# Kernel optimization log

Hardware: AMD Instinct MI355X
Metric: run time of the kernel (lower is better)

Reference implementation:

```python
import jax, jax.numpy as jnp
import numpy as np

B, C, Dz, Hh, Ww = 1, 128, 24, 24, 24
L = Dz * Hh * Ww
D_STATE = 16
D_CONV = 4
EXPAND = 2
D_INNER = EXPAND * C
DT_RANK = (C + 15) // 16  # ceil(d_model/16) = 8


def setup_inputs() -> dict:
    key = jax.random.key(0)
    ks = jax.random.split(key, 10)
    s = 0.02
    return {
        "x": jax.random.normal(ks[0], (B, C, Dz, Hh, Ww), dtype=jnp.float32),
        "ln_w": jnp.ones((C,), jnp.float32),
        "ln_b": jnp.zeros((C,), jnp.float32),
        "in_proj_w": s * jax.random.normal(ks[1], (2 * D_INNER, C), jnp.float32),
        "conv_w": s * jax.random.normal(ks[2], (D_INNER, D_CONV), jnp.float32),
        "conv_b": jnp.zeros((D_INNER,), jnp.float32),
        "x_proj_w": s * jax.random.normal(ks[3], (DT_RANK + 2 * D_STATE, D_INNER), jnp.float32),
        "dt_proj_w": s * jax.random.normal(ks[4], (D_INNER, DT_RANK), jnp.float32),
        "dt_proj_b": jax.random.uniform(ks[5], (D_INNER,), jnp.float32, -4.0, -2.0),
        "A_log": jnp.log(jnp.broadcast_to(jnp.arange(1, D_STATE + 1, dtype=jnp.float32), (D_INNER, D_STATE))),
        "D_param": jnp.ones((D_INNER,), jnp.float32),
        "out_proj_w": s * jax.random.normal(ks[6], (C, D_INNER), jnp.float32),
    }


def _mamba_forward(x, ln_w, ln_b, in_proj_w, conv_w, conv_b, x_proj_w,
                   dt_proj_w, dt_proj_b, A_log, D_param, out_proj_w):
    b, c, d, h, w = x.shape
    l = d * h * w
    tokens = x.reshape(b, c, l).transpose(0, 2, 1)  # (B,L,C)

    # LayerNorm over channel dim
    mu = jnp.mean(tokens, axis=-1, keepdims=True)
    var = jnp.var(tokens, axis=-1, keepdims=True)
    tn = (tokens - mu) * jax.lax.rsqrt(var + 1e-5) * ln_w + ln_b

    # in_proj -> x, z
    xz = jnp.einsum('blc,ec->ble', tn, in_proj_w)  # (B,L,2*d_inner)
    xs, z = jnp.split(xz, 2, axis=-1)

    # causal depthwise conv1d over L (kernel size D_CONV)
    xpad = jnp.pad(xs, ((0, 0), (D_CONV - 1, 0), (0, 0)))
    xc = conv_b
    xc = sum(xpad[:, k:k + l, :] * conv_w[:, k] for k in range(D_CONV)) + conv_b
    xa = jax.nn.silu(xc)  # (B,L,d_inner)

    # x_proj -> dt, B, C
    x_dbl = jnp.einsum('bld,ed->ble', xa, x_proj_w)
    dt_in = x_dbl[..., :DT_RANK]
    Bm = x_dbl[..., DT_RANK:DT_RANK + D_STATE]          # (B,L,d_state)
    Cm = x_dbl[..., DT_RANK + D_STATE:]                 # (B,L,d_state)
    dt = jax.nn.softplus(jnp.einsum('blr,dr->bld', dt_in, dt_proj_w) + dt_proj_b)

    A = -jnp.exp(A_log)  # (d_inner, d_state)

    def step(hst, inp):
        dt_t, B_t, C_t, x_t = inp  # (B,d_inner),(B,d_state),(B,d_state),(B,d_inner)
        dA = jnp.exp(dt_t[..., None] * A)                       # (B,d_inner,d_state)
        hst = dA * hst + (dt_t * x_t)[..., None] * B_t[:, None, :]
        y_t = jnp.einsum('bds,bs->bd', hst, C_t)
        return hst, y_t

    h0 = jnp.zeros((b, D_INNER, D_STATE), xa.dtype)
    xs_t = (dt.transpose(1, 0, 2), Bm.transpose(1, 0, 2), Cm.transpose(1, 0, 2), xa.transpose(1, 0, 2))
    _, ys = jax.lax.scan(step, h0, xs_t)
    y = ys.transpose(1, 0, 2) + xa * D_param  # (B,L,d_inner)

    y = y * jax.nn.silu(z)
    out = jnp.einsum('bld,cd->blc', y, out_proj_w)

    tokens = tokens + out
    return tokens.transpose(0, 2, 1).reshape(b, c, d, h, w)


def reference(x, ln_w, ln_b, in_proj_w, conv_w, conv_b, x_proj_w,
              dt_proj_w, dt_proj_b, A_log, D_param, out_proj_w):
    return _mamba_forward(x, ln_w, ln_b, in_proj_w, conv_w, conv_b, x_proj_w,
                          dt_proj_w, dt_proj_b, A_log, D_param, out_proj_w)
```

## Files before the change

### kernel.cpp

```cpp
#include <hip/hip_runtime.h>
#include <hip/hip_bf16.h>
#include <math.h>


constexpr int LQ = 13824;
constexpr int NC = 108;
constexpr int CH = 128;
constexpr int DI = 256;
constexpr int DS = 16;

typedef __attribute__((ext_vector_type(8))) short short8v;
typedef __attribute__((ext_vector_type(4))) float float4v;

__device__ __forceinline__ ushort f2bf(float f) {
  uint u = __float_as_uint(f);
  u += 0x7FFFu + ((u >> 16) & 1u);
  return (ushort)(u >> 16);
}
__device__ __forceinline__ float bf2f(ushort u) {
  return __uint_as_float(((uint)u) << 16);
}

template<int CTRL>
__device__ __forceinline__ float dpp_add(float x) {
  int y = __builtin_amdgcn_update_dpp(0, __float_as_int(x), CTRL, 0xF, 0xF, true);
  return x + __int_as_float(y);
}
__device__ __forceinline__ float dpp_reduce16(float t) {
  t = dpp_add<0xB1>(t);
  t = dpp_add<0x4E>(t);
  t = dpp_add<0x141>(t);
  t = dpp_add<0x140>(t);
  return t;
}

__global__ __launch_bounds__(256) void prep_w2(const float* __restrict__ w_in,
    const float* __restrict__ w_xp, const float* __restrict__ w_dt,
    const float* __restrict__ w_out,
    ushort* __restrict__ b_in, ushort* __restrict__ b_xp2, ushort* __restrict__ b_out) {
  int idx = blockIdx.x * 256 + threadIdx.x;
  if (idx < 65536) {
    b_in[idx] = f2bf(w_in[idx]);
  } else if (idx < 65536 + 8192) {
    int j = idx - 65536; int r = j >> 8, k = j & 255;
    b_xp2[j] = f2bf(w_xp[(8 + r) * 256 + k]);
  } else if (idx < 65536 + 8192 + 65536) {
    int j = idx - (65536 + 8192); int d = j >> 8, k = j & 255;
    float acc = 0.f;
    #pragma unroll
    for (int r = 0; r < 8; ++r) acc += w_dt[d * 8 + r] * w_xp[r * 256 + k];
    b_xp2[8192 + j] = f2bf(acc);
  } else if (idx < 65536 + 8192 + 65536 + 8192) {
    b_xp2[73728 + (idx - 139264)] = 0;
  } else if (idx < 180224) {
    int j = idx - 147456;
    b_out[j] = f2bf(w_out[j]);
  }
}

__global__ __launch_bounds__(256) void ln_t(const float* __restrict__ x,
    const float* __restrict__ lnw, const float* __restrict__ lnb,
    ushort* __restrict__ tn) {
  __shared__ float red[64][8];
  __shared__ float stat[64][2];
  __shared__ ushort T[64][136];
  const int t = threadIdx.x;
  const int l = t & 63, q = t >> 6;
  const int l0 = blockIdx.x * 64;
  float sum = 0.f, sq = 0.f;
  #pragma unroll 8
  for (int cc = 0; cc < 32; ++cc) {
    int c = q * 32 + cc;
    float v = x[(size_t)c * LQ + l0 + l];
    sum += v; sq += v * v;
  }
  red[l][q] = sum; red[l][4 + q] = sq;
  __syncthreads();
  if (t < 64) {
    float s  = red[t][0] + red[t][1] + red[t][2] + red[t][3];
    float s2 = red[t][4] + red[t][5] + red[t][6] + red[t][7];
    float mu = s * (1.f / 128.f);
    float var = s2 * (1.f / 128.f) - mu * mu;
    stat[t][0] = mu; stat[t][1] = rsqrtf(var + 1e-5f);
  }
  __syncthreads();
  float mu = stat[l][0], rs = stat[l][1];
  #pragma unroll 8
  for (int cc = 0; cc < 32; ++cc) {
    int c = q * 32 + cc;
    float v = x[(size_t)c * LQ + l0 + l];
    T[l][c] = f2bf((v - mu) * rs * lnw[c] + lnb[c]);
  }
  __syncthreads();
  int row = t >> 2, seg = t & 3;
  #pragma unroll
  for (int j = 0; j < 4; ++j) {
    short8v v = *(const short8v*)&T[row][seg * 32 + j * 8];
    *(short8v*)&tn[(size_t)(l0 + row) * 128 + seg * 32 + j * 8] = v;
  }
}

template<int K, int MV, int BSTR, int CSTR>
__global__ __launch_bounds__(256) void gemm_tok(
    const ushort* __restrict__ Wb,
    const ushort* __restrict__ Act,
    ushort* __restrict__ Out) {
  constexpr int KO = K / 8;
  __shared__ ushort As[64 * K];
  __shared__ ushort Bs[128 * 64];
  const int tid = threadIdx.x;
  const int l0 = blockIdx.x * 128;
  const int m0 = blockIdx.y * 64;
  #pragma unroll
  for (int i = 0; i < (64 * KO) / 256; ++i) {
    int cid = i * 256 + tid;
    int m = cid / KO, oct = cid % KO;
    short8v v = *(const short8v*)&Wb[(size_t)(m0 + m) * K + oct * 8];
    *(short8v*)&As[m * K + ((oct ^ (m & 7)) * 8)] = v;
  }
  float4v acc[4][2];
  #pragma unroll
  for (int a = 0; a < 4; ++a)
    #pragma unroll
    for (int b = 0; b < 2; ++b) acc[a][b] = (float4v)0.f;
  const int w = tid >> 6, lane = tid & 63;
  const int r = lane & 15, g = lane >> 4;
  for (int k0 = 0; k0 < K; k0 += 64) {
    __syncthreads();
    #pragma unroll
    for (int i = 0; i < 4; ++i) {
      int cid = i * 256 + tid;
      int l = cid >> 3, oct = cid & 7;
      short8v v = *(const short8v*)&Act[(size_t)(l0 + l) * BSTR + k0 + oct * 8];
      *(short8v*)&Bs[l * 64 + ((oct ^ (l & 7)) * 8)] = v;
    }
    __syncthreads();
    #pragma unroll
    for (int kk = 0; kk < 2; ++kk) {
      short8v af[4], bfv[2];
      int ko = (k0 >> 3) + kk * 4 + g;
      #pragma unroll
      for (int mf = 0; mf < 4; ++mf) {
        int row = mf * 16 + r;
        af[mf] = *(const short8v*)&As[row * K + ((ko ^ (row & 7)) * 8)];
      }
      int kob = kk * 4 + g;
      #pragma unroll
      for (int nf = 0; nf < 2; ++nf) {
        int row = w * 32 + nf * 16 + r;
        bfv[nf] = *(const short8v*)&Bs[row * 64 + ((kob ^ (row & 7)) * 8)];
      }
      #pragma unroll
      for (int mf = 0; mf < 4; ++mf)
        #pragma unroll
        for (int nf = 0; nf < 2; ++nf)
          acc[mf][nf] = __builtin_amdgcn_mfma_f32_16x16x32_bf16(af[mf], bfv[nf], acc[mf][nf], 0, 0, 0);
    }
  }
  __syncthreads();
  #pragma unroll
  for (int mf = 0; mf < 4; ++mf) {
    #pragma unroll
    for (int nf = 0; nf < 2; ++nf) {
      int l = w * 32 + nf * 16 + r;
      int m = mf * 16 + g * 4;
      ushort u0 = f2bf(acc[mf][nf][0]), u1 = f2bf(acc[mf][nf][1]);
      ushort u2 = f2bf(acc[mf][nf][2]), u3 = f2bf(acc[mf][nf][3]);
      uint2 pk = make_uint2((uint)u0 | ((uint)u1 << 16), (uint)u2 | ((uint)u3 << 16));
      int oct = (m >> 3) ^ (l & 7);
      *(uint2*)&Bs[l * 64 + oct * 8 + (g & 1) * 4] = pk;
    }
  }
  __syncthreads();
  #pragma unroll
  for (int i = 0; i < 4; ++i) {
    int cid = i * 256 + tid;
    int row = cid >> 3, oct = cid & 7;
    if (oct * 8 < MV) {
      short8v v = *(const short8v*)&Bs[row * 64 + ((oct ^ (row & 7)) * 8)];
      *(short8v*)&Out[(size_t)(l0 + row) * CSTR + m0 + oct * 8] = v;
    }
  }
}

__global__ __launch_bounds__(256) void gemm_out_k(
    const ushort* __restrict__ Wb,
    const ushort* __restrict__ Yg,
    const float* __restrict__ X,
    float* __restrict__ Out) {
  __shared__ ushort Ay[128 * 64];
  __shared__ ushort Bw[128 * 64];
  const int tid = threadIdx.x;
  const int l0 = blockIdx.x * 128;
  const int w = tid >> 6, lane = tid & 63;
  const int r = lane & 15, g = lane >> 4;
  const int lw = w >> 1, cw = w & 1;
  float4v acc[4][4];
  #pragma unroll
  for (int a = 0; a < 4; ++a)
    #pragma unroll
    for (int b = 0; b < 4; ++b) acc[a][b] = (float4v)0.f;
  for (int k0 = 0; k0 < 256; k0 += 64) {
    __syncthreads();
    #pragma unroll
    for (int i = 0; i < 4; ++i) {
      int cid = i * 256 + tid;
      int row = cid >> 3, oct = cid & 7;
      int k = k0 + oct * 8;
      int slab = k >> 4, rem = k & 15;
      short8v va = *(const short8v*)&Yg[((size_t)slab * LQ + l0 + row) * 16 + rem];
      *(short8v*)&Ay[row * 64 + ((oct ^ (row & 7)) * 8)] = va;
      short8v vb = *(const short8v*)&Wb[(size_t)row * 256 + k0 + oct * 8];
      *(short8v*)&Bw[row * 64 + ((oct ^ (row & 7)) * 8)] = vb;
    }
    __syncthreads();
    #pragma unroll
    for (int kk = 0; kk < 2; ++kk) {
      int ko = kk * 4 + g;
      short8v af[4], bfv[4];
      #pragma unroll
      for (int mf = 0; mf < 4; ++mf) {
        int row = lw * 64 + mf * 16 + r;
        af[mf] = *(const short8v*)&Ay[row * 64 + ((ko ^ (row & 7)) * 8)];
      }
      #pragma unroll
      for (int nf = 0; nf < 4; ++nf) {
        int row = cw * 64 + nf * 16 + r;
        bfv[nf] = *(const short8v*)&Bw[row * 64 + ((ko ^ (row & 7)) * 8)];
      }
      #pragma unroll
      for (int mf = 0; mf < 4; ++mf)
        #pragma unroll
        for (int nf = 0; nf < 4; ++nf)
          acc[mf][nf] = __builtin_amdgcn_mfma_f32_16x16x32_bf16(af[mf], bfv[nf], acc[mf][nf], 0, 0, 0);
    }
  }
  #pragma unroll
  for (int mf = 0; mf < 4; ++mf) {
    #pragma unroll
    for (int nf = 0; nf < 4; ++nf) {
      int c = cw * 64 + nf * 16 + r;
      int l = l0 + lw * 64 + mf * 16 + g * 4;
      size_t off = (size_t)c * LQ + l;
      float4 rv = *(const float4*)&X[off];
      float4 o = make_float4(acc[mf][nf][0] + rv.x, acc[mf][nf][1] + rv.y,
                             acc[mf][nf][2] + rv.z, acc[mf][nf][3] + rv.w);
      *(float4*)&Out[off] = o;
    }
  }
}

__global__ __launch_bounds__(256) void conv2(const ushort* __restrict__ xz,
    const float* __restrict__ cw, const float* __restrict__ cb,
    ushort* __restrict__ xa) {
  const int tid = threadIdx.x;
  const int d0 = (tid & 31) * 8;
  const int l0 = blockIdx.x * 32 + (tid >> 5) * 4;
  float w0[8], w1[8], w2[8], w3[8], bb[8];
  #pragma unroll
  for (int j = 0; j < 8; ++j) {
    float4 wv = *(const float4*)&cw[(d0 + j) * 4];
    w0[j] = wv.x; w1[j] = wv.y; w2[j] = wv.z; w3[j] = wv.w;
    bb[j] = cb[d0 + j];
  }
  float rbuf[7][8];
  #pragma unroll
  for (int t = 0; t < 7; ++t) {
    int ls = l0 - 3 + t;
    if (ls >= 0) {
      short8v v = *(const short8v*)&xz[(size_t)ls * 512 + d0];
      #pragma unroll
      for (int j = 0; j < 8; ++j) rbuf[t][j] = bf2f((ushort)v[j]);
    } else {
      #pragma unroll
      for (int j = 0; j < 8; ++j) rbuf[t][j] = 0.f;
    }
  }
  #pragma unroll
  for (int i = 0; i < 4; ++i) {
    short8v ov;
    #pragma unroll
    for (int j = 0; j < 8; ++j) {
      float acc = bb[j] + w0[j] * rbuf[i][j] + w1[j] * rbuf[i + 1][j]
                        + w2[j] * rbuf[i + 2][j] + w3[j] * rbuf[i + 3][j];
      ov[j] = (short)f2bf(acc / (1.f + __expf(-acc)));
    }
    *(short8v*)&xa[(size_t)(l0 + i) * 256 + d0] = ov;
  }
}

__global__ __launch_bounds__(256) void scan1(const ushort* __restrict__ xdbl,
    const ushort* __restrict__ xa, const float* __restrict__ bias,
    const float* __restrict__ A_log, float* __restrict__ Pc, float* __restrict__ Hc,
    ushort* __restrict__ yloc) {
  __shared__ uint  duL[128 * 17];
  __shared__ ushort bcL[128 * 40];
  __shared__ float ylds[128 * 18];
  const int tid = threadIdx.x;
  const int c = blockIdx.x, dg = blockIdx.y;
  const int l0 = c * CH;
  {
    const int row = tid >> 1, half = tid & 1;
    const ushort* xr = xdbl + (size_t)(l0 + row) * 320;
    short8v dl = *(const short8v*)(xr + 32 + dg * 16 + half * 8);
    short8v xv = *(const short8v*)(&xa[(size_t)(l0 + row) * 256 + dg * 16 + half * 8]);
    #pragma unroll
    for (int j = 0; j < 8; ++j) {
      float av = bf2f((ushort)dl[j]) + bias[dg * 16 + half * 8 + j];
      float sp = (av > 20.f) ? av : log1pf(__expf(av));
      float dx = sp * bf2f((ushort)xv[j]);
      duL[row * 17 + half * 8 + j] = (uint)f2bf(sp) | ((uint)f2bf(dx) << 16);
    }
    short8v bv = *(const short8v*)(xr + half * 8);
    short8v cv = *(const short8v*)(xr + 16 + half * 8);
    uint* bcu = (uint*)bcL;
    #pragma unroll
    for (int j = 0; j < 4; ++j) {
      bcu[row * 20 + half * 4 + j] =
          (uint)(ushort)bv[2 * j] | ((uint)(ushort)bv[2 * j + 1] << 16);
      bcu[row * 20 + 8 + half * 4 + j] =
          (uint)(ushort)cv[2 * j] | ((uint)(ushort)cv[2 * j + 1] << 16);
    }
  }
  __syncthreads();
  const int s = tid & 15, dloc = tid >> 4;
  const int d = dg * 16 + dloc;
  const float A = -__expf(A_log[d * DS + s]);
  float p = 1.f, h = 0.f;
  #pragma unroll 4
  for (int i = 0; i < CH; ++i) {
    uint pv = duL[i * 17 + dloc];
    float dtv = bf2f((ushort)(pv & 0xffffu));
    float dx  = bf2f((ushort)(pv >> 16));
    float a = __expf(dtv * A);
    p *= a;
    h = fmaf(a, h, dx * bf2f(bcL[i * 40 + s]));
    float t = dpp_reduce16(h * bf2f(bcL[i * 40 + 16 + s]));
    if (s == 0) ylds[i * 18 + dloc] = t;
  }
  int idx = (c * DI + d) * DS + s;
  Pc[idx] = p; Hc[idx] = h;
  __syncthreads();
  {
    const int row = tid >> 1, half = tid & 1;
    short8v ov;
    #pragma unroll
    for (int j = 0; j < 8; ++j) ov[j] = (short)f2bf(ylds[row * 18 + half * 8 + j]);
    *(short8v*)&yloc[((size_t)dg * LQ + l0 + row) * 16 + half * 8] = ov;
  }
}

__global__ __launch_bounds__(256) void scan_combine(const float* __restrict__ Pc,
    const float* __restrict__ Hc, float* __restrict__ Hin) {
  int t = blockIdx.x * 256 + threadIdx.x;
  float h = 0.f;
  for (int c = 0; c < NC; ++c) {
    Hin[c * 4096 + t] = h;
    h = Pc[c * 4096 + t] * h + Hc[c * 4096 + t];
  }
}

__global__ __launch_bounds__(256) void scan2(const ushort* __restrict__ xdbl,
    const ushort* __restrict__ xa, const ushort* __restrict__ xz,
    const float* __restrict__ bias, const float* __restrict__ A_log,
    const float* __restrict__ Dp, const float* __restrict__ Hin,
    ushort* __restrict__ yg) {
  __shared__ ushort dtL[128 * 18];
  __shared__ ushort cL[128 * 18];
  __shared__ float corr[128 * 18];
  const int tid = threadIdx.x;
  const int c = blockIdx.x, dg = blockIdx.y;
  const int l0 = c * CH;
  {
    const int row = tid >> 1, half = tid & 1;
    const ushort* xr = xdbl + (size_t)(l0 + row) * 320;
    short8v dl = *(const short8v*)(xr + 32 + dg * 16 + half * 8);
    short8v cv = *(const short8v*)(xr + 16 + half * 8);
    uint* dtu = (uint*)dtL;
    uint* cu  = (uint*)cL;
    ushort sp8[8];
    #pragma unroll
    for (int j = 0; j < 8; ++j) {
      float av = bf2f((ushort)dl[j]) + bias[dg * 16 + half * 8 + j];
      float sp = (av > 20.f) ? av : log1pf(__expf(av));
      sp8[j] = f2bf(sp);
    }
    #pragma unroll
    for (int j = 0; j < 4; ++j) {
      dtu[row * 9 + half * 4 + j] = (uint)sp8[2 * j] | ((uint)sp8[2 * j + 1] << 16);
      cu[row * 9 + half * 4 + j] =
          (uint)(ushort)cv[2 * j] | ((uint)(ushort)cv[2 * j + 1] << 16);
    }
  }
  __syncthreads();
  const int s = tid & 15, dloc = tid >> 4;
  const int d = dg * 16 + dloc;
  const float A = -__expf(A_log[d * DS + s]);
  const float hin = Hin[c * 4096 + d * DS + s];
  float S = 0.f;
  #pragma unroll 4
  for (int i = 0; i < CH; ++i) {
    S += bf2f(dtL[i * 18 + dloc]);
    float e = __expf(A * S);
    float t = dpp_reduce16((hin * e) * bf2f(cL[i * 18 + s]));
    if (s == 0) corr[i * 18 + dloc] = t;
  }
  __syncthreads();
  {
    const int row = tid >> 1, half = tid & 1;
    const size_t slab = ((size_t)dg * LQ + l0 + row) * 16 + half * 8;
    short8v yl = *(const short8v*)&yg[slab];
    short8v xv = *(const short8v*)&xa[(size_t)(l0 + row) * 256 + dg * 16 + half * 8];
    short8v zv = *(const short8v*)&xz[(size_t)(l0 + row) * 512 + 256 + dg * 16 + half * 8];
    short8v ov;
    #pragma unroll
    for (int j = 0; j < 8; ++j) {
      float val = bf2f((ushort)yl[j]) + corr[row * 18 + half * 8 + j]
                + bf2f((ushort)xv[j]) * Dp[dg * 16 + half * 8 + j];
      float zf = bf2f((ushort)zv[j]);
      val *= zf / (1.f + __expf(-zf));
      ov[j] = (short)f2bf(val);
    }
    *(short8v*)&yg[slab] = ov;
  }
}

extern "C" void kernel_launch(void* const* d_in, const int* in_sizes, int n_in,
                              void* d_out, int out_size, void* d_ws, size_t ws_size,
                              hipStream_t stream) {
  const float* x         = (const float*)d_in[0];
  const float* ln_w      = (const float*)d_in[1];
  const float* ln_b      = (const float*)d_in[2];
  const float* in_proj_w = (const float*)d_in[3];
  const float* conv_w    = (const float*)d_in[4];
  const float* conv_b    = (const float*)d_in[5];
  const float* x_proj_w  = (const float*)d_in[6];
  const float* dt_proj_w = (const float*)d_in[7];
  const float* dt_proj_b = (const float*)d_in[8];
  const float* A_log     = (const float*)d_in[9];
  const float* D_param   = (const float*)d_in[10];
  const float* out_proj_w= (const float*)d_in[11];
  float* out = (float*)d_out;

  char* ws = (char*)d_ws;
  ushort* wbf_in  = (ushort*)(ws + 0);
  ushort* wbf_xp2 = (ushort*)(ws + 131072);
  ushort* wbf_out = (ushort*)(ws + 294912);
  float*  Hin     = (float*)(ws + 360448);
  ushort* tn_t    = (ushort*)(ws + 2129920);
  float*  Pc      = (float*)(ws + 2129920);
  float*  Hc      = (float*)(ws + 3899392);
  ushort* xz_t    = (ushort*)(ws + 5668864);
  ushort* xa_t    = (ushort*)(ws + 19824640);
  ushort* xdbl_t  = (ushort*)(ws + 26902528);
  ushort* yg_t    = (ushort*)(ws + 35749888);

  prep_w2<<<704, 256, 0, stream>>>(in_proj_w, x_proj_w, dt_proj_w, out_proj_w,
                                   wbf_in, wbf_xp2, wbf_out);
  ln_t<<<LQ / 64, 256, 0, stream>>>(x, ln_w, ln_b, tn_t);
  gemm_tok<128, 64, 128, 512><<<dim3(NC, 8), 256, 0, stream>>>(wbf_in, tn_t, xz_t);
  conv2<<<LQ / 32, 256, 0, stream>>>(xz_t, conv_w, conv_b, xa_t);
  gemm_tok<256, 64, 256, 320><<<dim3(NC, 5), 256, 0, stream>>>(wbf_xp2, xa_t, xdbl_t);
  scan1<<<dim3(NC, 16), 256, 0, stream>>>(xdbl_t, xa_t, dt_proj_b, A_log, Pc, Hc, yg_t);
  scan_combine<<<16, 256, 0, stream>>>(Pc, Hc, Hin);
  scan2<<<dim3(NC, 16), 256, 0, stream>>>(xdbl_t, xa_t, xz_t, dt_proj_b, A_log,
                                          D_param, Hin, yg_t);
  gemm_out_k<<<NC, 256, 0, stream>>>(wbf_out, yg_t, x, out);
}
```

Baseline: 207.2 us.

## Remap scan threads to four states per lane and split out-proj GEMM over channels

The chunked selective scan now gives each thread four state elements for one channel, so the cross-lane reduction needs only a quad DPP step instead of a 16-lane one. Each block covers 64 channels in two 64-step stages, and B/C are staged as fp32 in shared memory. The per-chunk decay product is replaced by a cumulative dt sum that scan_combine turns back into exp(A*S). The output GEMM is also split across two column blocks to double its grid. This trades fewer, larger scan blocks (432 instead of 1728) for less shuffle and LDS traffic per step, which may lower occupancy on the scan kernels.

```diff
diff --git a/kernel.cpp b/kernel.cpp
--- a/kernel.cpp
+++ b/kernel.cpp
@@ -26,12 +26,13 @@
   int y = __builtin_amdgcn_update_dpp(0, __float_as_int(x), CTRL, 0xF, 0xF, true);
   return x + __int_as_float(y);
 }
-__device__ __forceinline__ float dpp_reduce16(float t) {
+__device__ __forceinline__ float quad_reduce(float t) {
   t = dpp_add<0xB1>(t);
   t = dpp_add<0x4E>(t);
-  t = dpp_add<0x141>(t);
-  t = dpp_add<0x140>(t);
   return t;
+}
+__device__ __forceinline__ float softplus_f(float x) {
+  return (x > 20.f) ? x : log1pf(__expf(x));
 }
 
 __global__ __launch_bounds__(256) void prep_w2(const float* __restrict__ w_in,
@@ -189,15 +190,15 @@
     const float* __restrict__ X,
     float* __restrict__ Out) {
   __shared__ ushort Ay[128 * 64];
-  __shared__ ushort Bw[128 * 64];
+  __shared__ ushort Bw[64 * 64];
   const int tid = threadIdx.x;
   const int l0 = blockIdx.x * 128;
+  const int c0 = blockIdx.y * 64;
   const int w = tid >> 6, lane = tid & 63;
   const int r = lane & 15, g = lane >> 4;
-  const int lw = w >> 1, cw = w & 1;
-  float4v acc[4][4];
-  #pragma unroll
-  for (int a = 0; a < 4; ++a)
+  float4v acc[2][4];
+  #pragma unroll
+  for (int a = 0; a < 2; ++a)
     #pragma unroll
     for (int b = 0; b < 4; ++b) acc[a][b] = (float4v)0.f;
   for (int k0 = 0; k0 < 256; k0 += 64) {
@@ -210,37 +211,42 @@
       int slab = k >> 4, rem = k & 15;
       short8v va = *(const short8v*)&Yg[((size_t)slab * LQ + l0 + row) * 16 + rem];
       *(short8v*)&Ay[row * 64 + ((oct ^ (row & 7)) * 8)] = va;
-      short8v vb = *(const short8v*)&Wb[(size_t)row * 256 + k0 + oct * 8];
+    }
+    #pragma unroll
+    for (int i = 0; i < 2; ++i) {
+      int cid = i * 256 + tid;
+      int row = cid >> 3, oct = cid & 7;
+      short8v vb = *(const short8v*)&Wb[(size_t)(c0 + row) * 256 + k0 + oct * 8];
       *(short8v*)&Bw[row * 64 + ((oct ^ (row & 7)) * 8)] = vb;
     }
     __syncthreads();
     #pragma unroll
     for (int kk = 0; kk < 2; ++kk) {
       int ko = kk * 4 + g;
-      short8v af[4], bfv[4];
-      #pragma unroll
-      for (int mf = 0; mf < 4; ++mf) {
-        int row = lw * 64 + mf * 16 + r;
+      short8v af[2], bfv[4];
+      #pragma unroll
+      for (int mf = 0; mf < 2; ++mf) {
+        int row = w * 32 + mf * 16 + r;
         af[mf] = *(const short8v*)&Ay[row * 64 + ((ko ^ (row & 7)) * 8)];
       }
       #pragma unroll
       for (int nf = 0; nf < 4; ++nf) {
-        int row = cw * 64 + nf * 16 + r;
+        int row = nf * 16 + r;
         bfv[nf] = *(const short8v*)&Bw[row * 64 + ((ko ^ (row & 7)) * 8)];
       }
       #pragma unroll
-      for (int mf = 0; mf < 4; ++mf)
+      for (int mf = 0; mf < 2; ++mf)
         #pragma unroll
         for (int nf = 0; nf < 4; ++nf)
           acc[mf][nf] = __builtin_amdgcn_mfma_f32_16x16x32_bf16(af[mf], bfv[nf], acc[mf][nf], 0, 0, 0);
     }
   }
   #pragma unroll
-  for (int mf = 0; mf < 4; ++mf) {
+  for (int mf = 0; mf < 2; ++mf) {
     #pragma unroll
     for (int nf = 0; nf < 4; ++nf) {
-      int c = cw * 64 + nf * 16 + r;
-      int l = l0 + lw * 64 + mf * 16 + g * 4;
+      int c = c0 + nf * 16 + r;
+      int l = l0 + w * 32 + mf * 16 + g * 4;
       size_t off = (size_t)c * LQ + l;
       float4 rv = *(const float4*)&X[off];
       float4 o = make_float4(acc[mf][nf][0] + rv.x, acc[mf][nf][1] + rv.y,
@@ -291,72 +297,103 @@
 
 __global__ __launch_bounds__(256) void scan1(const ushort* __restrict__ xdbl,
     const ushort* __restrict__ xa, const float* __restrict__ bias,
-    const float* __restrict__ A_log, float* __restrict__ Pc, float* __restrict__ Hc,
+    const float* __restrict__ A_log, float* __restrict__ Stot, float* __restrict__ Hc,
     ushort* __restrict__ yloc) {
-  __shared__ uint  duL[128 * 17];
-  __shared__ ushort bcL[128 * 40];
-  __shared__ float ylds[128 * 18];
+  __shared__ uint  duL[64 * 64];
+  __shared__ float bcL[64 * 32];
+  __shared__ ushort ylds[64 * 72];
   const int tid = threadIdx.x;
   const int c = blockIdx.x, dg = blockIdx.y;
-  const int l0 = c * CH;
-  {
-    const int row = tid >> 1, half = tid & 1;
-    const ushort* xr = xdbl + (size_t)(l0 + row) * 320;
-    short8v dl = *(const short8v*)(xr + 32 + dg * 16 + half * 8);
-    short8v xv = *(const short8v*)(&xa[(size_t)(l0 + row) * 256 + dg * 16 + half * 8]);
-    #pragma unroll
-    for (int j = 0; j < 8; ++j) {
-      float av = bf2f((ushort)dl[j]) + bias[dg * 16 + half * 8 + j];
-      float sp = (av > 20.f) ? av : log1pf(__expf(av));
-      float dx = sp * bf2f((ushort)xv[j]);
-      duL[row * 17 + half * 8 + j] = (uint)f2bf(sp) | ((uint)f2bf(dx) << 16);
-    }
-    short8v bv = *(const short8v*)(xr + half * 8);
-    short8v cv = *(const short8v*)(xr + 16 + half * 8);
-    uint* bcu = (uint*)bcL;
-    #pragma unroll
-    for (int j = 0; j < 4; ++j) {
-      bcu[row * 20 + half * 4 + j] =
-          (uint)(ushort)bv[2 * j] | ((uint)(ushort)bv[2 * j + 1] << 16);
-      bcu[row * 20 + 8 + half * 4 + j] =
-          (uint)(ushort)cv[2 * j] | ((uint)(ushort)cv[2 * j + 1] << 16);
-    }
-  }
-  __syncthreads();
-  const int s = tid & 15, dloc = tid >> 4;
-  const int d = dg * 16 + dloc;
-  const float A = -__expf(A_log[d * DS + s]);
-  float p = 1.f, h = 0.f;
-  #pragma unroll 4
-  for (int i = 0; i < CH; ++i) {
-    uint pv = duL[i * 17 + dloc];
-    float dtv = bf2f((ushort)(pv & 0xffffu));
-    float dx  = bf2f((ushort)(pv >> 16));
-    float a = __expf(dtv * A);
-    p *= a;
-    h = fmaf(a, h, dx * bf2f(bcL[i * 40 + s]));
-    float t = dpp_reduce16(h * bf2f(bcL[i * 40 + 16 + s]));
-    if (s == 0) ylds[i * 18 + dloc] = t;
-  }
-  int idx = (c * DI + d) * DS + s;
-  Pc[idx] = p; Hc[idx] = h;
-  __syncthreads();
-  {
-    const int row = tid >> 1, half = tid & 1;
-    short8v ov;
-    #pragma unroll
-    for (int j = 0; j < 8; ++j) ov[j] = (short)f2bf(ylds[row * 18 + half * 8 + j]);
-    *(short8v*)&yloc[((size_t)dg * LQ + l0 + row) * 16 + half * 8] = ov;
-  }
-}
-
-__global__ __launch_bounds__(256) void scan_combine(const float* __restrict__ Pc,
-    const float* __restrict__ Hc, float* __restrict__ Hin) {
+  const int dloc = tid >> 2, sq = tid & 3;
+  const int d = dg * 64 + dloc;
+  float4v A, h;
+  #pragma unroll
+  for (int k = 0; k < 4; ++k) {
+    A[k] = -__expf(A_log[d * 16 + sq * 4 + k]);
+    h[k] = 0.f;
+  }
+  float S = 0.f;
+  for (int stg = 0; stg < 2; ++stg) {
+    const int lb = c * CH + stg * 64;
+    __syncthreads();
+    {
+      const int doff = dg * 64 + sq * 16;
+      const ushort* xr = xdbl + (size_t)(lb + dloc) * 320 + 32 + doff;
+      const ushort* xar = xa + (size_t)(lb + dloc) * 256 + doff;
+      short8v d0 = *(const short8v*)xr;
+      short8v d1 = *(const short8v*)(xr + 8);
+      short8v x0 = *(const short8v*)xar;
+      short8v x1 = *(const short8v*)(xar + 8);
+      uint pk[16];
+      #pragma unroll
+      for (int j = 0; j < 8; ++j) {
+        float sp = softplus_f(bf2f((ushort)d0[j]) + bias[doff + j]);
+        pk[j] = (uint)f2bf(sp) | ((uint)f2bf(sp * bf2f((ushort)x0[j])) << 16);
+        float sp2 = softplus_f(bf2f((ushort)d1[j]) + bias[doff + 8 + j]);
+        pk[8 + j] = (uint)f2bf(sp2) | ((uint)f2bf(sp2 * bf2f((ushort)x1[j])) << 16);
+      }
+      uint4* dst = (uint4*)&duL[dloc * 64 + sq * 16];
+      #pragma unroll
+      for (int j = 0; j < 4; ++j)
+        dst[j] = make_uint4(pk[4 * j], pk[4 * j + 1], pk[4 * j + 2], pk[4 * j + 3]);
+    }
+    if (tid < 128) {
+      int row = tid >> 1, half = tid & 1;
+      const ushort* xr = xdbl + (size_t)(lb + row) * 320;
+      short8v bv = *(const short8v*)(xr + half * 8);
+      short8v cv = *(const short8v*)(xr + 16 + half * 8);
+      float* bd = &bcL[row * 32 + half * 8];
+      float* cd = &bcL[row * 32 + 16 + half * 8];
+      #pragma unroll
+      for (int j = 0; j < 8; ++j) {
+        bd[j] = bf2f((ushort)bv[j]);
+        cd[j] = bf2f((ushort)cv[j]);
+      }
+    }
+    __syncthreads();
+    #pragma unroll 4
+    for (int i = 0; i < 64; ++i) {
+      uint pv = duL[i * 64 + dloc];
+      float dtv = __uint_as_float(pv << 16);
+      float dxv = __uint_as_float(pv & 0xffff0000u);
+      S += dtv;
+      float4v Bv = *(const float4v*)&bcL[i * 32 + sq * 4];
+      float4v Cv = *(const float4v*)&bcL[i * 32 + 16 + sq * 4];
+      float t = 0.f;
+      #pragma unroll
+      for (int k = 0; k < 4; ++k) {
+        float a = __expf(dtv * A[k]);
+        h[k] = fmaf(a, h[k], dxv * Bv[k]);
+        t = fmaf(h[k], Cv[k], t);
+      }
+      t = quad_reduce(t);
+      if (sq == 0) ylds[i * 72 + dloc] = f2bf(t);
+    }
+    __syncthreads();
+    {
+      int slab = tid >> 6, row = tid & 63;
+      short8v v0 = *(const short8v*)&ylds[row * 72 + slab * 16];
+      short8v v1 = *(const short8v*)&ylds[row * 72 + slab * 16 + 8];
+      ushort* dst = &yloc[((size_t)(dg * 4 + slab) * LQ + lb + row) * 16];
+      *(short8v*)dst = v0;
+      *(short8v*)(dst + 8) = v1;
+    }
+  }
+  *(float4*)&Hc[(size_t)(c * 256 + d) * 16 + sq * 4] = make_float4(h[0], h[1], h[2], h[3]);
+  if (sq == 0) Stot[c * 256 + d] = S;
+}
+
+__global__ __launch_bounds__(256) void scan_combine(const float* __restrict__ Stot,
+    const float* __restrict__ Hc, const float* __restrict__ A_log,
+    float* __restrict__ Hin) {
   int t = blockIdx.x * 256 + threadIdx.x;
+  int d = t >> 4;
+  float A = -__expf(A_log[t]);
   float h = 0.f;
   for (int c = 0; c < NC; ++c) {
     Hin[c * 4096 + t] = h;
-    h = Pc[c * 4096 + t] * h + Hc[c * 4096 + t];
+    float a = __expf(A * Stot[c * 256 + d]);
+    h = a * h + Hc[c * 4096 + t];
   }
 }
 
@@ -365,63 +402,99 @@
     const float* __restrict__ bias, const float* __restrict__ A_log,
     const float* __restrict__ Dp, const float* __restrict__ Hin,
     ushort* __restrict__ yg) {
-  __shared__ ushort dtL[128 * 18];
-  __shared__ ushort cL[128 * 18];
-  __shared__ float corr[128 * 18];
+  __shared__ uint  dtp[32 * 64];
+  __shared__ float cL[64 * 16];
+  __shared__ float corr[64 * 68];
   const int tid = threadIdx.x;
   const int c = blockIdx.x, dg = blockIdx.y;
-  const int l0 = c * CH;
+  const int dloc = tid >> 2, sq = tid & 3;
+  const int d = dg * 64 + dloc;
+  float4v A, hin;
+  #pragma unroll
+  for (int k = 0; k < 4; ++k) A[k] = -__expf(A_log[d * 16 + sq * 4 + k]);
   {
-    const int row = tid >> 1, half = tid & 1;
-    const ushort* xr = xdbl + (size_t)(l0 + row) * 320;
-    short8v dl = *(const short8v*)(xr + 32 + dg * 16 + half * 8);
-    short8v cv = *(const short8v*)(xr + 16 + half * 8);
-    uint* dtu = (uint*)dtL;
-    uint* cu  = (uint*)cL;
-    ushort sp8[8];
-    #pragma unroll
-    for (int j = 0; j < 8; ++j) {
-      float av = bf2f((ushort)dl[j]) + bias[dg * 16 + half * 8 + j];
-      float sp = (av > 20.f) ? av : log1pf(__expf(av));
-      sp8[j] = f2bf(sp);
-    }
-    #pragma unroll
-    for (int j = 0; j < 4; ++j) {
-      dtu[row * 9 + half * 4 + j] = (uint)sp8[2 * j] | ((uint)sp8[2 * j + 1] << 16);
-      cu[row * 9 + half * 4 + j] =
-          (uint)(ushort)cv[2 * j] | ((uint)(ushort)cv[2 * j + 1] << 16);
-    }
-  }
-  __syncthreads();
-  const int s = tid & 15, dloc = tid >> 4;
-  const int d = dg * 16 + dloc;
-  const float A = -__expf(A_log[d * DS + s]);
-  const float hin = Hin[c * 4096 + d * DS + s];
+    float4 hv = *(const float4*)&Hin[(size_t)(c * 256 + d) * 16 + sq * 4];
+    hin[0] = hv.x; hin[1] = hv.y; hin[2] = hv.z; hin[3] = hv.w;
+  }
   float S = 0.f;
-  #pragma unroll 4
-  for (int i = 0; i < CH; ++i) {
-    S += bf2f(dtL[i * 18 + dloc]);
-    float e = __expf(A * S);
-    float t = dpp_reduce16((hin * e) * bf2f(cL[i * 18 + s]));
-    if (s == 0) corr[i * 18 + dloc] = t;
-  }
-  __syncthreads();
-  {
-    const int row = tid >> 1, half = tid & 1;
-    const size_t slab = ((size_t)dg * LQ + l0 + row) * 16 + half * 8;
-    short8v yl = *(const short8v*)&yg[slab];
-    short8v xv = *(const short8v*)&xa[(size_t)(l0 + row) * 256 + dg * 16 + half * 8];
-    short8v zv = *(const short8v*)&xz[(size_t)(l0 + row) * 512 + 256 + dg * 16 + half * 8];
-    short8v ov;
-    #pragma unroll
-    for (int j = 0; j < 8; ++j) {
-      float val = bf2f((ushort)yl[j]) + corr[row * 18 + half * 8 + j]
-                + bf2f((ushort)xv[j]) * Dp[dg * 16 + half * 8 + j];
-      float zf = bf2f((ushort)zv[j]);
-      val *= zf / (1.f + __expf(-zf));
-      ov[j] = (short)f2bf(val);
-    }
-    *(short8v*)&yg[slab] = ov;
+  for (int stg = 0; stg < 2; ++stg) {
+    const int lb = c * CH + stg * 64;
+    __syncthreads();
+    {
+      int rp = tid >> 3, seg = tid & 7;
+      const int doff = dg * 64 + seg * 8;
+      const ushort* xr0 = xdbl + (size_t)(lb + 2 * rp) * 320 + 32 + doff;
+      short8v e0 = *(const short8v*)xr0;
+      short8v e1 = *(const short8v*)(xr0 + 320);
+      uint pk[8];
+      #pragma unroll
+      for (int j = 0; j < 8; ++j) {
+        float spe = softplus_f(bf2f((ushort)e0[j]) + bias[doff + j]);
+        float spo = softplus_f(bf2f((ushort)e1[j]) + bias[doff + j]);
+        pk[j] = (uint)f2bf(spe) | ((uint)f2bf(spo) << 16);
+      }
+      uint4* dst = (uint4*)&dtp[rp * 64 + seg * 8];
+      dst[0] = make_uint4(pk[0], pk[1], pk[2], pk[3]);
+      dst[1] = make_uint4(pk[4], pk[5], pk[6], pk[7]);
+    }
+    if (tid < 128) {
+      int row = tid >> 1, half = tid & 1;
+      short8v cv = *(const short8v*)(xdbl + (size_t)(lb + row) * 320 + 16 + half * 8);
+      float* cd = &cL[row * 16 + half * 8];
+      #pragma unroll
+      for (int j = 0; j < 8; ++j) cd[j] = bf2f((ushort)cv[j]);
+    }
+    __syncthreads();
+    #pragma unroll 2
+    for (int i2 = 0; i2 < 32; ++i2) {
+      uint pv = dtp[i2 * 64 + dloc];
+      #pragma unroll
+      for (int par = 0; par < 2; ++par) {
+        float dtv = (par == 0) ? __uint_as_float(pv << 16)
+                               : __uint_as_float(pv & 0xffff0000u);
+        S += dtv;
+        int i = i2 * 2 + par;
+        float4v Cv = *(const float4v*)&cL[i * 16 + sq * 4];
+        float t = 0.f;
+        #pragma unroll
+        for (int k = 0; k < 4; ++k)
+          t = fmaf(__expf(A[k] * S), hin[k] * Cv[k], t);
+        t = quad_reduce(t);
+        if (sq == 0) corr[i * 68 + dloc] = t;
+      }
+    }
+    __syncthreads();
+    {
+      int slab = tid >> 6, row = tid & 63;
+      const int doff = dg * 64 + slab * 16;
+      size_t sl = ((size_t)(dg * 4 + slab) * LQ + lb + row) * 16;
+      short8v y0 = *(const short8v*)&yg[sl];
+      short8v y1 = *(const short8v*)&yg[sl + 8];
+      const ushort* xav = xa + (size_t)(lb + row) * 256 + doff;
+      short8v x0 = *(const short8v*)xav;
+      short8v x1 = *(const short8v*)(xav + 8);
+      const ushort* zvp = xz + (size_t)(lb + row) * 512 + 256 + doff;
+      short8v z0 = *(const short8v*)zvp;
+      short8v z1 = *(const short8v*)(zvp + 8);
+      float4 c0 = *(const float4*)&corr[row * 68 + slab * 16];
+      float4 c1 = *(const float4*)&corr[row * 68 + slab * 16 + 4];
+      float4 c2 = *(const float4*)&corr[row * 68 + slab * 16 + 8];
+      float4 c3 = *(const float4*)&corr[row * 68 + slab * 16 + 12];
+      float cr[16] = {c0.x, c0.y, c0.z, c0.w, c1.x, c1.y, c1.z, c1.w,
+                      c2.x, c2.y, c2.z, c2.w, c3.x, c3.y, c3.z, c3.w};
+      short8v o0, o1;
+      #pragma unroll
+      for (int j = 0; j < 8; ++j) {
+        float v0 = bf2f((ushort)y0[j]) + cr[j] + bf2f((ushort)x0[j]) * Dp[doff + j];
+        float zf0 = bf2f((ushort)z0[j]);
+        o0[j] = (short)f2bf(v0 * (zf0 / (1.f + __expf(-zf0))));
+        float v1 = bf2f((ushort)y1[j]) + cr[8 + j] + bf2f((ushort)x1[j]) * Dp[doff + 8 + j];
+        float zf1 = bf2f((ushort)z1[j]);
+        o1[j] = (short)f2bf(v1 * (zf1 / (1.f + __expf(-zf1))));
+      }
+      *(short8v*)&yg[sl] = o0;
+      *(short8v*)&yg[sl + 8] = o1;
+    }
   }
 }
 
@@ -448,7 +521,7 @@
   ushort* wbf_out = (ushort*)(ws + 294912);
   float*  Hin     = (float*)(ws + 360448);
   ushort* tn_t    = (ushort*)(ws + 2129920);
-  float*  Pc      = (float*)(ws + 2129920);
+  float*  Stot    = (float*)(ws + 2129920);
   float*  Hc      = (float*)(ws + 3899392);
   ushort* xz_t    = (ushort*)(ws + 5668864);
   ushort* xa_t    = (ushort*)(ws + 19824640);
@@ -461,9 +534,9 @@
   gemm_tok<128, 64, 128, 512><<<dim3(NC, 8), 256, 0, stream>>>(wbf_in, tn_t, xz_t);
   conv2<<<LQ / 32, 256, 0, stream>>>(xz_t, conv_w, conv_b, xa_t);
   gemm_tok<256, 64, 256, 320><<<dim3(NC, 5), 256, 0, stream>>>(wbf_xp2, xa_t, xdbl_t);
-  scan1<<<dim3(NC, 16), 256, 0, stream>>>(xdbl_t, xa_t, dt_proj_b, A_log, Pc, Hc, yg_t);
-  scan_combine<<<16, 256, 0, stream>>>(Pc, Hc, Hin);
-  scan2<<<dim3(NC, 16), 256, 0, stream>>>(xdbl_t, xa_t, xz_t, dt_proj_b, A_log,
-                                          D_param, Hin, yg_t);
-  gemm_out_k<<<NC, 256, 0, stream>>>(wbf_out, yg_t, x, out);
-}
+  scan1<<<dim3(NC, 4), 256, 0, stream>>>(xdbl_t, xa_t, dt_proj_b, A_log, Stot, Hc, yg_t);
+  scan_combine<<<16, 256, 0, stream>>>(Stot, Hc, A_log, Hin);
+  scan2<<<dim3(NC, 4), 256, 0, stream>>>(xdbl_t, xa_t, xz_t, dt_proj_b, A_log,
+                                         D_param, Hin, yg_t);
+  gemm_out_k<<<dim3(NC, 2), 256, 0, stream>>>(wbf_out, yg_t, x, out);
+}
```

New measurement: 202.5 us. 2.3% less time.
